# Optimization experiments

Hardware: AMD Instinct MI355X
Metric: run time of the kernel (lower is better)

## Reference

```python
import jax, jax.numpy as jnp
import numpy as np

N_NODES = 10000
N_EDGES = 160000
D = 128        # embedding_dim = in/out channels
E_DIM = 32     # edge feature dim
HEADS = 3
N_ETYPES = 64
ROUNDS = 2     # num_message_rounds
NEG_SLOPE = 0.2


def _lookup_maxnorm(table, idx):
    # torch Embedding(max_norm=1): rows with L2 norm > 1 are renormalized to norm 1
    v = table[idx]
    n = jnp.linalg.norm(v, axis=-1, keepdims=True)
    return v / jnp.maximum(n, 1.0)


def _edge_gat(x, src, dst, edge_attr, weight, att, euw, bias):
    # x: [N, D]; src/dst: [E] (self loops included); edge_attr: [E, E_DIM]
    N = x.shape[0]
    H = HEADS
    C = weight.shape[1] // H
    xh = (x @ weight).reshape(N, H, C)                 # [N, H, C]
    x_j = xh[src]                                      # gather source nodes  [E, H, C]
    x_i = xh[dst]                                      # gather target nodes  [E, H, C]
    ea = jnp.broadcast_to(edge_attr[:, None, :], (src.shape[0], H, edge_attr.shape[-1]))
    xj_cat = jnp.concatenate([x_j, ea], axis=-1)       # [E, H, C+E_DIM]
    # attention logits: (cat(x_i, x_j, e) * att).sum(-1)
    alpha = jnp.sum(jnp.concatenate([x_i, xj_cat], axis=-1) * att, axis=-1)  # [E, H]
    alpha = jax.nn.leaky_relu(alpha, NEG_SLOPE)
    # scatter-softmax over incoming edges of each dst node (stable)
    m = jax.ops.segment_max(alpha, dst, num_segments=N)        # [N, H]
    a = jnp.exp(alpha - m[dst])
    denom = jax.ops.segment_sum(a, dst, num_segments=N)        # [N, H]
    a = a / denom[dst]
    # weighted scatter-add aggregate
    aggr = jax.ops.segment_sum(xj_cat * a[..., None], dst, num_segments=N)  # [N, H, C+E_DIM]
    return aggr.mean(axis=1) @ euw + bias                       # [N, C]


def setup_inputs() -> dict:
    key = jax.random.key(0)
    ks = jax.random.split(key, 13)
    x_idx = jnp.arange(N_NODES, dtype=jnp.int32)
    src = jax.random.randint(ks[0], (N_EDGES,), 0, N_NODES, dtype=jnp.int32)
    off = jax.random.randint(ks[1], (N_EDGES,), 1, N_NODES, dtype=jnp.int32)
    dst = (src + off) % N_NODES    # guaranteed self-loop-free
    edge_index = jnp.stack([src, dst])
    edge_attr_idx = jax.random.randint(ks[2], (N_EDGES,), 0, N_ETYPES, dtype=jnp.int32)
    def g(k, shape):
        return jax.random.normal(k, shape, jnp.float32) * np.float32(np.sqrt(2.0 / sum(shape)))
    node_emb = g(ks[3], (N_NODES, D))
    edge_emb = g(ks[4], (N_ETYPES, E_DIM))
    w1 = g(ks[5], (D, HEADS * D))
    att1 = g(ks[6], (1, HEADS, 2 * D + E_DIM))
    euw1 = g(ks[7], (D + E_DIM, D))
    b1 = jnp.zeros((D,), jnp.float32)
    w2 = g(ks[8], (D, HEADS * D))
    att2 = g(ks[9], (1, HEADS, 2 * D + E_DIM))
    euw2 = g(ks[10], (D + E_DIM, D))
    b2 = jnp.zeros((D,), jnp.float32)
    return dict(x_idx=x_idx, edge_index=edge_index, edge_attr_idx=edge_attr_idx,
                node_emb=node_emb, edge_emb=edge_emb,
                w1=w1, att1=att1, euw1=euw1, b1=b1,
                w2=w2, att2=att2, euw2=euw2, b2=b2)


def reference(x_idx, edge_index, edge_attr_idx, node_emb, edge_emb,
              w1, att1, euw1, b1, w2, att2, euw2, b2):
    N = node_emb.shape[0]
    src0, dst0 = edge_index[0], edge_index[1]
    loop = jnp.arange(N, dtype=src0.dtype)
    src = jnp.concatenate([src0, loop])
    dst = jnp.concatenate([dst0, loop])
    x = _lookup_maxnorm(node_emb, x_idx)               # [N, D]
    ea = edge_emb[edge_attr_idx]                       # [E0, E_DIM]
    ea_full = jnp.concatenate([ea, jnp.zeros((N, ea.shape[-1]), ea.dtype)], axis=0)
    for _ in range(ROUNDS):
        # eval mode: dropout is identity
        x = jax.nn.elu(_edge_gat(x, src, dst, ea_full, w1, att1, euw1, b1))
        x = _edge_gat(x, src, dst, ea_full, w2, att2, euw2, b2)
    return x
```

## Files before the change

### kernel.cpp

```cpp
#include <hip/hip_runtime.h>
#include <hip/hip_bf16.h>

typedef __hip_bfloat16 bf16;
typedef __attribute__((ext_vector_type(8))) short short8;
typedef __attribute__((ext_vector_type(4))) float f32x4;
typedef __attribute__((ext_vector_type(4), aligned(4))) int i32x4u;
typedef __attribute__((ext_vector_type(4))) int i32x4;

__device__ __forceinline__ float b2f(bf16 v) { return __bfloat162float(v); }
__device__ __forceinline__ float2 i2f2(int w) {
  float lo = __uint_as_float(((unsigned)w) << 16);
  float hi = __uint_as_float(((unsigned)w) & 0xFFFF0000u);
  return make_float2(lo, hi);
}
__device__ __forceinline__ unsigned f2bfb(float f) {
  unsigned u = __float_as_uint(f);
  unsigned r = 0x7FFFu + ((u >> 16) & 1u);
  return (u + r) >> 16;
}
__device__ __forceinline__ unsigned pk2(float a, float b) {
  return f2bfb(a) | (f2bfb(b) << 16);
}
__device__ __forceinline__ float ldv(const void* p, int i, int f) {
  return f ? ((const float*)p)[i] : b2f(((const bf16*)p)[i]);
// ... 120 lines not shown
  if (hi > N) hi = N;
  int s = 0;
  for (int i = lo; i < hi; ++i) s += counts[i] + 1;
  int lane = t & 63, wv = t >> 6;
  int incl = s;
#pragma unroll
  for (int d = 1; d < 64; d <<= 1) {
    int u = __shfl_up(incl, d);
    if (lane >= d) incl += u;
  }
  if (lane == 63) wsum[wv] = incl;
  __syncthreads();
  if (t == 0) {
    int run = 0;
#pragma unroll
    for (int w = 0; w < 16; ++w) { int c = wsum[w]; wsum[w] = run; run += c; }
  }
  __syncthreads();
  int run = incl - s + wsum[wv];
  for (int i = lo; i < hi; ++i) {
    int c = counts[i] + 1;
    row_ptr[i] = run;
    counts[i] = run;
    run += c;
  }
  if (t == 1023) row_ptr[N] = run;
}

__global__ __launch_bounds__(256) void scatter_kernel(
    const int* __restrict__ src, const int* __restrict__ dst,
    const int* __restrict__ et, int* __restrict__ cursor,
    int* __restrict__ packed, int E0, int N) {
  int E = E0 + N;
  int i = blockIdx.x * blockDim.x + threadIdx.x;
  if (i < E0) {
    int d = dst[i];
    if ((unsigned)d >= (unsigned)N) d = 0;
    int p = atomicAdd(&cursor[d], 1);
    if ((unsigned)p >= (unsigned)E) p = 0;
    int t = et[i] & 63;
    packed[p] = (src[i] & 0xFFFF) | (t << 16);
  } else if (i < E) {
    int n = i - E0;
    int p = atomicAdd(&cursor[n], 1);
    if ((unsigned)p >= (unsigned)E) p = 0;
    packed[p] = (n & 0xFFFF) | (64 << 16);
  }
}

__global__ __launch_bounds__(384) void gemm_xh_s_mfma(
    const bf16* __restrict__ x, const bf16* __restrict__ WT,
    const float* __restrict__ attf, bf16* __restrict__ xh,
    float* __restrict__ s_i, float* __restrict__ s_j, int N) {
  __shared__ bf16 stage[32 * SH];
  __shared__ float lds_i[6][32];
  __shared__ float lds_j[6][32];
  int wave = threadIdx.x >> 6, lane = threadIdx.x & 63;
  int row_base = blockIdx.x * 32;
  int quad = lane >> 4, r16 = lane & 15;
  int rowA = row_base + r16;      if (rowA >= N) rowA = N - 1;
  int rowB = row_base + 16 + r16; if (rowB >= N) rowB = N - 1;
  const short8* apA = (const short8*)(x + (size_t)rowA * 128 + quad * 8);
  const short8* apB = (const short8*)(x + (size_t)rowB * 128 + quad * 8);
  short8 aA[4], aB[4];
#pragma unroll
  for (int kk = 0; kk < 4; ++kk) { aA[kk] = apA[kk * 4]; aB[kk] = apB[kk * 4]; }

  float piA[4] = {0.f, 0.f, 0.f, 0.f}, pjA[4] = {0.f, 0.f, 0.f, 0.f};
  float piB[4] = {0.f, 0.f, 0.f, 0.f}, pjB[4] = {0.f, 0.f, 0.f, 0.f};
#pragma unroll
  for (int j = 0; j < 4; ++j) {
    int col = wave * 64 + j * 16 + r16;
    const short8* bp = (const short8*)(WT + (size_t)col * 128 + quad * 8);
    short8 b[4];
#pragma unroll
    for (int kk = 0; kk < 4; ++kk) b[kk] = bp[kk * 4];
    f32x4 accA = {0.f, 0.f, 0.f, 0.f};
    f32x4 accB = {0.f, 0.f, 0.f, 0.f};
#pragma unroll
    for (int kk = 0; kk < 4; ++kk) {
      accA = __builtin_amdgcn_mfma_f32_16x16x32_bf16(aA[kk], b[kk], accA, 0, 0, 0);
      accB = __builtin_amdgcn_mfma_f32_16x16x32_bf16(aB[kk], b[kk], accB, 0, 0, 0);
    }
    int h = col >> 7, fi = col & 127, pair = fi >> 1, sub = fi & 1;
    int base = pair * 6 + h * 2 + sub;
#pragma unroll
    for (int r = 0; r < 4; ++r) {
      stage[(quad * 4 + r) * SH + base] = __float2bfloat16(accA[r]);
      stage[(16 + quad * 4 + r) * SH + base] = __float2bfloat16(accB[r]);
    }
    float ai = attf[h * 288 + fi];
    float aj = attf[h * 288 + 128 + fi];
#pragma unroll
    for (int r = 0; r < 4; ++r) {
      piA[r] = fmaf(accA[r], ai, piA[r]);
      pjA[r] = fmaf(accA[r], aj, pjA[r]);
      piB[r] = fmaf(accB[r], ai, piB[r]);
      pjB[r] = fmaf(accB[r], aj, pjB[r]);
    }
  }
#pragma unroll
  for (int d = 1; d < 16; d <<= 1) {
#pragma unroll
    for (int r = 0; r < 4; ++r) {
      piA[r] += __shfl_xor(piA[r], d);
      pjA[r] += __shfl_xor(pjA[r], d);
      piB[r] += __shfl_xor(piB[r], d);
      pjB[r] += __shfl_xor(pjB[r], d);
    }
  }
  if (r16 == 0) {
#pragma unroll
    for (int r = 0; r < 4; ++r) {
      lds_i[wave][quad * 4 + r] = piA[r];
      lds_j[wave][quad * 4 + r] = pjA[r];
      lds_i[wave][16 + quad * 4 + r] = piB[r];
      lds_j[wave][16 + quad * 4 + r] = pjB[r];
    }
  }
  __syncthreads();
  int m = threadIdx.x;
  if (m < 96) {
    int h = m / 32, r = m % 32;
    int node = row_base + r;
    if (node < N) s_i[node * 3 + h] = lds_i[2 * h][r] + lds_i[2 * h + 1][r];
  } else if (m < 192) {
    int tt = m - 96;
    int h = tt / 32, r = tt % 32;
    int node = row_base + r;
    if (node < N) s_j[node * 3 + h] = lds_j[2 * h][r] + lds_j[2 * h + 1][r];
  }
#pragma unroll
  for (int k = 0; k < 4; ++k) {
    int c = threadIdx.x + k * 384;
    int r = c / 48, o = c % 48;
    int node = row_base + r;
    if (node < N)
      *(i32x4*)(xh + (size_t)node * 384 + o * 8) =
          *(const i32x4*)(stage + r * SH + o * 8);
  }
}

__global__ __launch_bounds__(384) void fox_kernel(
    const bf16* __restrict__ aggr, const bf16* __restrict__ euwT,
    const float* __restrict__ biasf, int do_elu,
    const bf16* __restrict__ WT, const float* __restrict__ attf,
    bf16* __restrict__ xh, float* __restrict__ s_i, float* __restrict__ s_j,
    int N) {
  __shared__ bf16 xtile[16][136];
  __shared__ bf16 stage[16 * SH];
  __shared__ float lds_i[6][16];
  __shared__ float lds_j[6][16];
  int wave = threadIdx.x >> 6, lane = threadIdx.x & 63;
  int quad = lane >> 4, r16 = lane & 15;
  int row_base = blockIdx.x * 16;
  int row = row_base + r16; if (row >= N) row = N - 1;

  const short8* ap = (const short8*)(aggr + (size_t)row * 160 + quad * 8);
  short8 aa[5];
#pragma unroll
  for (int kk = 0; kk < 5; ++kk) aa[kk] = ap[kk * 4];
  for (int t = wave; t < 8; t += 6) {
    int col = t * 16 + r16;
    const short8* bp = (const short8*)(euwT + (size_t)col * 160 + quad * 8);
    f32x4 acc = {0.f, 0.f, 0.f, 0.f};
#pragma unroll
    for (int kk = 0; kk < 5; ++kk)
      acc = __builtin_amdgcn_mfma_f32_16x16x32_bf16(aa[kk], bp[kk * 4], acc, 0, 0, 0);
    float bv = biasf[col];
#pragma unroll
    for (int r = 0; r < 4; ++r) {
      float v = acc[r] + bv;
      if (do_elu) v = v > 0.0f ? v : expm1f(v);
      xtile[quad * 4 + r][col] = __float2bfloat16(v);
    }
  }
  __syncthreads();

  short8 a[4];
#pragma unroll
  for (int kk = 0; kk < 4; ++kk)
    a[kk] = *(const short8*)(&xtile[r16][quad * 8 + kk * 32]);

  float pi_r[4] = {0.f, 0.f, 0.f, 0.f};
  float pj_r[4] = {0.f, 0.f, 0.f, 0.f};
#pragma unroll
  for (int j = 0; j < 4; ++j) {
    int col = wave * 64 + j * 16 + r16;
    const short8* bp = (const short8*)(WT + (size_t)col * 128 + quad * 8);
    f32x4 acc = {0.f, 0.f, 0.f, 0.f};
#pragma unroll
    for (int kk = 0; kk < 4; ++kk)
      acc = __builtin_amdgcn_mfma_f32_16x16x32_bf16(a[kk], bp[kk * 4], acc, 0, 0, 0);
    int h = col >> 7, fi = col & 127, pair = fi >> 1, sub = fi & 1;
    int base = pair * 6 + h * 2 + sub;
#pragma unroll
    for (int r = 0; r < 4; ++r)
      stage[(quad * 4 + r) * SH + base] = __float2bfloat16(acc[r]);
    float ai = attf[h * 288 + fi];
    float aj = attf[h * 288 + 128 + fi];
#pragma unroll
    for (int r = 0; r < 4; ++r) {
      pi_r[r] = fmaf(acc[r], ai, pi_r[r]);
      pj_r[r] = fmaf(acc[r], aj, pj_r[r]);
    }
  }
#pragma unroll
  for (int d = 1; d < 16; d <<= 1) {
#pragma unroll
    for (int r = 0; r < 4; ++r) {
      pi_r[r] += __shfl_xor(pi_r[r], d);
      pj_r[r] += __shfl_xor(pj_r[r], d);
    }
  }
  if (r16 == 0) {
#pragma unroll
    for (int r = 0; r < 4; ++r) {
      lds_i[wave][quad * 4 + r] = pi_r[r];
      lds_j[wave][quad * 4 + r] = pj_r[r];
    }
  }
  __syncthreads();
  int m = threadIdx.x;
  if (m < 48) {
    int h = m / 16, r = m % 16;
    int node = row_base + r;
    if (node < N) s_i[node * 3 + h] = lds_i[2 * h][r] + lds_i[2 * h + 1][r];
  } else if (m < 96) {
    int tt = m - 48;
    int h = tt / 16, r = tt % 16;
    int node = row_base + r;
    if (node < N) s_j[node * 3 + h] = lds_j[2 * h][r] + lds_j[2 * h + 1][r];
  }
#pragma unroll
  for (int k = 0; k < 2; ++k) {
    int c = threadIdx.x + k * 384;
    int r = c / 48, o = c % 48;
    int node = row_base + r;
    if (node < N)
      *(i32x4*)(xh + (size_t)node * 384 + o * 8) =
          *(const i32x4*)(stage + r * SH + o * 8);
  }
}

__global__ __launch_bounds__(256) void edge_aggr_kernel(
    const int* __restrict__ xh_i, const float* __restrict__ s_i,
    const float* __restrict__ s_j, const float* __restrict__ s_et,
    const float2* __restrict__ eef2, const int* __restrict__ row_ptr,
    const int* __restrict__ packed, unsigned* __restrict__ aggr_u,
    int N, int E) {
  __shared__ float lds[2][512];
  int wid = threadIdx.x >> 6, lane = threadIdx.x & 63;
  int nodeLocal = wid >> 1, w = wid & 1;
  int n0 = blockIdx.x * 2 + nodeLocal;
  int n = n0 < N ? n0 : N - 1;
  int start = row_ptr[n], end = row_ptr[n + 1];
  if (start < 0) start = 0;
  if (start > E) start = E;
  if (end < start) end = start;
  if (end > E) end = E;
  int deg = end - start;
  float si0 = s_i[n * 3 + 0], si1 = s_i[n * 3 + 1], si2 = s_i[n * 3 + 2];

  float p0r = 0.f, p1r = 0.f, p2r = 0.f;
  int pkr = 0;
  float dp0 = 0.0f, dp1 = 0.0f, dp2 = 0.0f;
  int slot = 2 * lane + w;
  if (slot < deg) {
    int p = packed[start + slot];
    int s = p & 0xFFFF; if (s >= N) s = N - 1;
    int t = (p >> 16) & 127; if (t > 64) t = 64;
    float a0 = si0 + s_j[s * 3 + 0] + s_et[t * 3 + 0];
    float a1 = si1 + s_j[s * 3 + 1] + s_et[t * 3 + 1];
    float a2 = si2 + s_j[s * 3 + 2] + s_et[t * 3 + 2];
    a0 = a0 > 0.0f ? a0 : 0.2f * a0;
    a1 = a1 > 0.0f ? a1 : 0.2f * a1;
    a2 = a2 > 0.0f ? a2 : 0.2f * a2;
    a0 = fminf(fmaxf(a0, -60.0f), 60.0f);
    a1 = fminf(fmaxf(a1, -60.0f), 60.0f);
    a2 = fminf(fmaxf(a2, -60.0f), 60.0f);
    p0r = __expf(a0); p1r = __expf(a1); p2r = __expf(a2);
    dp0 = p0r; dp1 = p1r; dp2 = p2r;
    pkr = s | (t << 16);
  }
#pragma unroll
  for (int d = 32; d > 0; d >>= 1) {
    dp0 += __shfl_xor(dp0, d);
    dp1 += __shfl_xor(dp1, d);
    dp2 += __shfl_xor(dp2, d);
  }
  float d0 = dp0, d1 = dp1, d2 = dp2;

  float2 ax0 = make_float2(0.f, 0.f), ax1 = ax0, ax2 = ax0;
  float2 ae0 = ax0, ae1 = ax0, ae2 = ax0;
  int capped = deg < 128 ? deg : 128;
  int cnt = (capped > w) ? ((capped - w + 1) >> 1) : 0;

  {
    int j = 0;
    for (; j + 2 <= cnt; j += 2) {
      int pkA = __shfl(pkr, j), pkB = __shfl(pkr, j + 1);
      float qA0 = __shfl(p0r, j), qB0 = __shfl(p0r, j + 1);
      float qA1 = __shfl(p1r, j), qB1 = __shfl(p1r, j + 1);
      float qA2 = __shfl(p2r, j), qB2 = __shfl(p2r, j + 1);
      int sA = pkA & 0xFFFF, tA = pkA >> 16;
      int sB = pkB & 0xFFFF, tB = pkB >> 16;
      i32x4u qA = *(const i32x4u*)(xh_i + (size_t)sA * 192 + lane * 3);
      i32x4u qB = *(const i32x4u*)(xh_i + (size_t)sB * 192 + lane * 3);
      float2 vA0 = i2f2(qA.x), vA1 = i2f2(qA.y), vA2 = i2f2(qA.z);
      float2 vB0 = i2f2(qB.x), vB1 = i2f2(qB.y), vB2 = i2f2(qB.z);
      ax0.x = fmaf(qA0, vA0.x, ax0.x); ax0.y = fmaf(qA0, vA0.y, ax0.y);
      ax1.x = fmaf(qA1, vA1.x, ax1.x); ax1.y = fmaf(qA1, vA1.y, ax1.y);
      ax2.x = fmaf(qA2, vA2.x, ax2.x); ax2.y = fmaf(qA2, vA2.y, ax2.y);
      ax0.x = fmaf(qB0, vB0.x, ax0.x); ax0.y = fmaf(qB0, vB0.y, ax0.y);
      ax1.x = fmaf(qB1, vB1.x, ax1.x); ax1.y = fmaf(qB1, vB1.y, ax1.y);
      ax2.x = fmaf(qB2, vB2.x, ax2.x); ax2.y = fmaf(qB2, vB2.y, ax2.y);
      if (lane < 16) {
        if (tA != 64) {
          float2 ev = eef2[tA * 16 + lane];
          ae0.x = fmaf(qA0, ev.x, ae0.x); ae0.y = fmaf(qA0, ev.y, ae0.y);
          ae1.x = fmaf(qA1, ev.x, ae1.x); ae1.y = fmaf(qA1, ev.y, ae1.y);
          ae2.x = fmaf(qA2, ev.x, ae2.x); ae2.y = fmaf(qA2, ev.y, ae2.y);
        }
        if (tB != 64) {
          float2 ev = eef2[tB * 16 + lane];
          ae0.x = fmaf(qB0, ev.x, ae0.x); ae0.y = fmaf(qB0, ev.y, ae0.y);
          ae1.x = fmaf(qB1, ev.x, ae1.x); ae1.y = fmaf(qB1, ev.y, ae1.y);
          ae2.x = fmaf(qB2, ev.x, ae2.x); ae2.y = fmaf(qB2, ev.y, ae2.y);
        }
      }
    }
    if (j < cnt) {
      int pkA = __shfl(pkr, j);
      float qA0 = __shfl(p0r, j), qA1 = __shfl(p1r, j), qA2 = __shfl(p2r, j);
      int sA = pkA & 0xFFFF, tA = pkA >> 16;
      i32x4u qA = *(const i32x4u*)(xh_i + (size_t)sA * 192 + lane * 3);
      float2 vA0 = i2f2(qA.x), vA1 = i2f2(qA.y), vA2 = i2f2(qA.z);
      ax0.x = fmaf(qA0, vA0.x, ax0.x); ax0.y = fmaf(qA0, vA0.y, ax0.y);
      ax1.x = fmaf(qA1, vA1.x, ax1.x); ax1.y = fmaf(qA1, vA1.y, ax1.y);
      ax2.x = fmaf(qA2, vA2.x, ax2.x); ax2.y = fmaf(qA2, vA2.y, ax2.y);
      if (lane < 16 && tA != 64) {
        float2 ev = eef2[tA * 16 + lane];
        ae0.x = fmaf(qA0, ev.x, ae0.x); ae0.y = fmaf(qA0, ev.y, ae0.y);
        ae1.x = fmaf(qA1, ev.x, ae1.x); ae1.y = fmaf(qA1, ev.y, ae1.y);
        ae2.x = fmaf(qA2, ev.x, ae2.x); ae2.y = fmaf(qA2, ev.y, ae2.y);
      }
    }
  }

  if (w == 0) {
    for (int e = start + 128; e < end; ++e) {
      int p = packed[e];
      int s = p & 0xFFFF; if (s >= N) s = N - 1;
      int t = (p >> 16) & 127; if (t > 64) t = 64;
      float a0 = si0 + s_j[s * 3 + 0] + s_et[t * 3 + 0];
      float a1 = si1 + s_j[s * 3 + 1] + s_et[t * 3 + 1];
      float a2 = si2 + s_j[s * 3 + 2] + s_et[t * 3 + 2];
      a0 = a0 > 0.0f ? a0 : 0.2f * a0;
      a1 = a1 > 0.0f ? a1 : 0.2f * a1;
      a2 = a2 > 0.0f ? a2 : 0.2f * a2;
      a0 = fminf(fmaxf(a0, -60.0f), 60.0f);
      a1 = fminf(fmaxf(a1, -60.0f), 60.0f);
      a2 = fminf(fmaxf(a2, -60.0f), 60.0f);
      float p0 = __expf(a0), p1 = __expf(a1), p2 = __expf(a2);
      d0 += p0; d1 += p1; d2 += p2;
      i32x4u q = *(const i32x4u*)(xh_i + (size_t)s * 192 + lane * 3);
      float2 v0 = i2f2(q.x), v1 = i2f2(q.y), v2 = i2f2(q.z);
      ax0.x = fmaf(p0, v0.x, ax0.x); ax0.y = fmaf(p0, v0.y, ax0.y);
      ax1.x = fmaf(p1, v1.x, ax1.x); ax1.y = fmaf(p1, v1.y, ax1.y);
      ax2.x = fmaf(p2, v2.x, ax2.x); ax2.y = fmaf(p2, v2.y, ax2.y);
      if (t != 64 && lane < 16) {
        float2 ev = eef2[t * 16 + lane];
        ae0.x = fmaf(p0, ev.x, ae0.x); ae0.y = fmaf(p0, ev.y, ae0.y);
        ae1.x = fmaf(p1, ev.x, ae1.x); ae1.y = fmaf(p1, ev.y, ae1.y);
        ae2.x = fmaf(p2, ev.x, ae2.x); ae2.y = fmaf(p2, ev.y, ae2.y);
      }
    }
  }

  float* L = lds[nodeLocal];
  if (w == 1) {
    L[lane * 2 + 0] = ax0.x;       L[lane * 2 + 1] = ax0.y;
    L[128 + lane * 2 + 0] = ax1.x; L[128 + lane * 2 + 1] = ax1.y;
    L[256 + lane * 2 + 0] = ax2.x; L[256 + lane * 2 + 1] = ax2.y;
    if (lane < 16) {
      L[384 + lane * 2 + 0] = ae0.x; L[384 + lane * 2 + 1] = ae0.y;
      L[416 + lane * 2 + 0] = ae1.x; L[416 + lane * 2 + 1] = ae1.y;
      L[448 + lane * 2 + 0] = ae2.x; L[448 + lane * 2 + 1] = ae2.y;
    }
    if (lane == 0) { L[480] = d0; L[481] = d1; L[482] = d2; }
  }
  __syncthreads();
  if (w == 0 && n0 < N) {
    ax0.x += L[lane * 2 + 0];       ax0.y += L[lane * 2 + 1];
    ax1.x += L[128 + lane * 2 + 0]; ax1.y += L[128 + lane * 2 + 1];
    ax2.x += L[256 + lane * 2 + 0]; ax2.y += L[256 + lane * 2 + 1];
    if (lane < 16) {
      ae0.x += L[384 + lane * 2 + 0]; ae0.y += L[384 + lane * 2 + 1];
      ae1.x += L[416 + lane * 2 + 0]; ae1.y += L[416 + lane * 2 + 1];
      ae2.x += L[448 + lane * 2 + 0]; ae2.y += L[448 + lane * 2 + 1];
    }
    d0 += L[480]; d1 += L[481]; d2 += L[482];
    const float third = 1.0f / 3.0f;
    float i0 = third / fmaxf(d0, 1e-30f);
    float i1 = third / fmaxf(d1, 1e-30f);
    float i2 = third / fmaxf(d2, 1e-30f);
    aggr_u[(size_t)n0 * 80 + lane] =
        pk2(ax0.x * i0 + ax1.x * i1 + ax2.x * i2,
            ax0.y * i0 + ax1.y * i1 + ax2.y * i2);
    if (lane < 16)
      aggr_u[(size_t)n0 * 80 + 64 + lane] =
          pk2(ae0.x * i0 + ae1.x * i1 + ae2.x * i2,
              ae0.y * i0 + ae1.y * i1 + ae2.y * i2);
  }
}

__global__ __launch_bounds__(256) void gemm_out_mfma(
    const bf16* __restrict__ aggr, const bf16* __restrict__ euwT,
    const float* __restrict__ biasf, void* __restrict__ dout,
    const int* __restrict__ flag, int N) {
  int wave = threadIdx.x >> 6, lane = threadIdx.x & 63;
  int row_base = blockIdx.x * 16;
  int col_base = blockIdx.y * 64 + wave * 16;
  int quad = lane >> 4, r16 = lane & 15;
  int row = row_base + r16; if (row >= N) row = N - 1;
  int col = col_base + r16;
  f32x4 acc = {0.f, 0.f, 0.f, 0.f};
  const short8* ap = (const short8*)(aggr + (size_t)row * 160 + quad * 8);
  const short8* bp = (const short8*)(euwT + (size_t)col * 160 + quad * 8);
#pragma unroll
  for (int kk = 0; kk < 5; ++kk) {
    short8 a = ap[kk * 4];
    short8 b = bp[kk * 4];
    acc = __builtin_amdgcn_mfma_f32_16x16x32_bf16(a, b, acc, 0, 0, 0);
  }
  float bv = biasf[col];
  int f = *flag;
#pragma unroll
  for (int r = 0; r < 4; ++r) {
    int node = row_base + quad * 4 + r;
    if (node < N) {
      float v = acc[r] + bv;
      if (f) ((float*)dout)[(size_t)node * 128 + col] = v;
      else   ((bf16*)dout)[(size_t)node * 128 + col] = __float2bfloat16(v);
    }
  }
}

extern "C" void kernel_launch(void* const* d_in, const int* in_sizes, int n_in,
                              void* d_out, int out_size, void* d_ws, size_t ws_size,
                              hipStream_t stream) {
  const int* x_idx = (const int*)d_in[0];
  const int* edge_index = (const int*)d_in[1];
  const int* edge_attr_idx = (const int*)d_in[2];

  int N = in_sizes[0];
  int E0 = in_sizes[1] / 2;
  int E = E0 + N;
  const int* src = edge_index;
  const int* dst = edge_index + E0;

  size_t off = 0;
  char* base = (char*)d_ws;
  auto carve = [&](size_t bytes) -> void* {
    void* p = base + off;
    off += (bytes + 255) & ~(size_t)255;
    return p;
  };
  int* flag     = (int*)carve(256);
  int* counts   = (int*)carve((size_t)N * 4);
  int* row_ptr  = (int*)carve((size_t)(N + 1) * 4);
  int* packed   = (int*)carve((size_t)E * 4);
  float* s_i    = (float*)carve((size_t)N * 3 * 4);
  float* s_j    = (float*)carve((size_t)N * 3 * 4);
  float* s_et   = (float*)carve(2 * 65 * 3 * 4);
  float* eef    = (float*)carve(2048 * 4);
  float* att1f  = (float*)carve(864 * 4);
  float* att2f  = (float*)carve(864 * 4);
  float* b1f    = (float*)carve(128 * 4);
  float* b2f_   = (float*)carve(128 * 4);
  bf16* WT1     = (bf16*)carve(49152 * 2);
  bf16* WT2     = (bf16*)carve(49152 * 2);
  bf16* euT1    = (bf16*)carve(20480 * 2);
  bf16* euT2    = (bf16*)carve(20480 * 2);
  bf16* xh      = (bf16*)carve((size_t)N * 384 * 2 + 64);
  bf16* aggr    = (bf16*)carve((size_t)N * 160 * 2);
  bf16* xb      = (bf16*)d_out;
  (void)n_in; (void)out_size; (void)ws_size;

  wconv_kernel<<<(143296 + N + 255) / 256, 256, 0, stream>>>(
      d_in[4], d_in[5], d_in[6], d_in[7], d_in[8], d_in[9], d_in[10], d_in[11],
      d_in[12], flag, eef, att1f, att2f, b1f, b2f_, WT1, WT2, euT1, euT2,
      s_et, counts, N);
  int nb4 = (N + 3) / 4;
  prep_kernel<<<nb4, 256, 0, stream>>>(x_idx, d_in[3], flag, xb, counts, dst,
                                       E0, N);
  scan_kernel<<<1, 1024, 0, stream>>>(counts, row_ptr, N);
  scatter_kernel<<<(E + 255) / 256, 256, 0, stream>>>(src, dst, edge_attr_idx,
                                                      counts, packed, E0, N);

  int nrb16 = (N + 15) / 16;
  int nrb32 = (N + 31) / 32;
  int nb2 = (N + 1) / 2;

  gemm_xh_s_mfma<<<nrb32, 384, 0, stream>>>(xb, WT1, att1f, xh, s_i, s_j, N);
  edge_aggr_kernel<<<nb2, 256, 0, stream>>>(
      (const int*)xh, s_i, s_j, s_et, (const float2*)eef,
      row_ptr, packed, (unsigned*)aggr, N, E);
  fox_kernel<<<nrb16, 384, 0, stream>>>(aggr, euT1, b1f, 1, WT2, att2f,
                                        xh, s_i, s_j, N);
  edge_aggr_kernel<<<nb2, 256, 0, stream>>>(
      (const int*)xh, s_i, s_j, s_et + 195, (const float2*)eef,
      row_ptr, packed, (unsigned*)aggr, N, E);
  fox_kernel<<<nrb16, 384, 0, stream>>>(aggr, euT2, b2f_, 0, WT1, att1f,
                                        xh, s_i, s_j, N);
  edge_aggr_kernel<<<nb2, 256, 0, stream>>>(
      (const int*)xh, s_i, s_j, s_et, (const float2*)eef,
      row_ptr, packed, (unsigned*)aggr, N, E);
  fox_kernel<<<nrb16, 384, 0, stream>>>(aggr, euT1, b1f, 1, WT2, att2f,
                                        xh, s_i, s_j, N);
  edge_aggr_kernel<<<nb2, 256, 0, stream>>>(
      (const int*)xh, s_i, s_j, s_et + 195, (const float2*)eef,
      row_ptr, packed, (unsigned*)aggr, N, E);
  gemm_out_mfma<<<dim3(nrb16, 2), 256, 0, stream>>>(aggr, euT2, b2f_,
                                                    d_out, flag, N);
}
```

Baseline: 315.3 us.

## Fuse edge aggregation with following node GEMMs into one kernel per layer

Merges the per-node edge softmax aggregation with the subsequent euw projection, ELU and next-layer W GEMM (or the final output GEMM) into a single kernel. The aggregated features stay in shared memory instead of round-tripping through a global aggr buffer. To make this safe, xh and the s_i/s_j buffers are double-buffered across layers. Each wave now handles two nodes sequentially with one wave per node instead of two waves per node, which may reduce latency hiding on high-degree nodes and lowers grid parallelism.

```diff
diff --git a/kernel.cpp b/kernel.cpp
--- a/kernel.cpp
+++ b/kernel.cpp
@@ -196,7 +196,7 @@
     const bf16* __restrict__ x, const bf16* __restrict__ WT,
     const float* __restrict__ attf, bf16* __restrict__ xh,
     float* __restrict__ s_i, float* __restrict__ s_j, int N) {
-  __shared__ bf16 stage[32 * SH];
+  __shared__ __align__(16) bf16 stage[32 * SH];
   __shared__ float lds_i[6][32];
   __shared__ float lds_j[6][32];
   int wave = threadIdx.x >> 6, lane = threadIdx.x & 63;
@@ -285,27 +285,169 @@
   }
 }
 
-__global__ __launch_bounds__(384) void fox_kernel(
-    const bf16* __restrict__ aggr, const bf16* __restrict__ euwT,
-    const float* __restrict__ biasf, int do_elu,
-    const bf16* __restrict__ WT, const float* __restrict__ attf,
-    bf16* __restrict__ xh, float* __restrict__ s_i, float* __restrict__ s_j,
-    int N) {
+#define AGGR_NODE_BODY(n_, start_, deg_)                                      \
+  float2 ax0 = make_float2(0.f, 0.f), ax1 = ax0, ax2 = ax0;                   \
+  float2 ae0 = ax0, ae1 = ax0, ae2 = ax0;                                     \
+  float d0 = 0.f, d1 = 0.f, d2 = 0.f;                                         \
+  {                                                                           \
+    float si0 = s_i[(n_) * 3 + 0], si1 = s_i[(n_) * 3 + 1],                   \
+          si2 = s_i[(n_) * 3 + 2];                                            \
+    for (int c0 = 0; c0 < (deg_); c0 += 64) {                                 \
+      int mm = (deg_) - c0; if (mm > 64) mm = 64;                             \
+      float p0r = 0.f, p1r = 0.f, p2r = 0.f; int pkr = 0;                     \
+      if (lane < mm) {                                                        \
+        int p = packed[(start_) + c0 + lane];                                 \
+        int s = p & 0xFFFF; if (s >= N) s = N - 1;                            \
+        int t = (p >> 16) & 127; if (t > 64) t = 64;                          \
+        float a0 = si0 + s_j[s * 3 + 0] + s_et[t * 3 + 0];                    \
+        float a1 = si1 + s_j[s * 3 + 1] + s_et[t * 3 + 1];                    \
+        float a2 = si2 + s_j[s * 3 + 2] + s_et[t * 3 + 2];                    \
+        a0 = a0 > 0.0f ? a0 : 0.2f * a0;                                      \
+        a1 = a1 > 0.0f ? a1 : 0.2f * a1;                                      \
+        a2 = a2 > 0.0f ? a2 : 0.2f * a2;                                      \
+        a0 = fminf(fmaxf(a0, -60.0f), 60.0f);                                 \
+        a1 = fminf(fmaxf(a1, -60.0f), 60.0f);                                 \
+        a2 = fminf(fmaxf(a2, -60.0f), 60.0f);                                 \
+        p0r = __expf(a0); p1r = __expf(a1); p2r = __expf(a2);                 \
+        pkr = s | (t << 16);                                                  \
+      }                                                                       \
+      float dp0 = p0r, dp1 = p1r, dp2 = p2r;                                  \
+      _Pragma("unroll")                                                       \
+      for (int d = 32; d > 0; d >>= 1) {                                      \
+        dp0 += __shfl_xor(dp0, d);                                            \
+        dp1 += __shfl_xor(dp1, d);                                            \
+        dp2 += __shfl_xor(dp2, d);                                            \
+      }                                                                       \
+      d0 += dp0; d1 += dp1; d2 += dp2;                                        \
+      int j = 0;                                                              \
+      for (; j + 4 <= mm; j += 4) {                                           \
+        int pkA = __shfl(pkr, j), pkB = __shfl(pkr, j + 1);                   \
+        int pkC = __shfl(pkr, j + 2), pkD = __shfl(pkr, j + 3);               \
+        float qA0 = __shfl(p0r, j), qB0 = __shfl(p0r, j + 1);                 \
+        float qC0 = __shfl(p0r, j + 2), qD0 = __shfl(p0r, j + 3);             \
+        float qA1 = __shfl(p1r, j), qB1 = __shfl(p1r, j + 1);                 \
+        float qC1 = __shfl(p1r, j + 2), qD1 = __shfl(p1r, j + 3);             \
+        float qA2 = __shfl(p2r, j), qB2 = __shfl(p2r, j + 1);                 \
+        float qC2 = __shfl(p2r, j + 2), qD2 = __shfl(p2r, j + 3);             \
+        int sA = pkA & 0xFFFF, tA = pkA >> 16;                                \
+        int sB = pkB & 0xFFFF, tB = pkB >> 16;                                \
+        int sC = pkC & 0xFFFF, tC = pkC >> 16;                                \
+        int sD = pkD & 0xFFFF, tD = pkD >> 16;                                \
+        i32x4u qA = *(const i32x4u*)(xh_i + (size_t)sA * 192 + lane * 3);     \
+        i32x4u qB = *(const i32x4u*)(xh_i + (size_t)sB * 192 + lane * 3);     \
+        i32x4u qC = *(const i32x4u*)(xh_i + (size_t)sC * 192 + lane * 3);     \
+        i32x4u qD = *(const i32x4u*)(xh_i + (size_t)sD * 192 + lane * 3);     \
+        float2 vA0 = i2f2(qA.x), vA1 = i2f2(qA.y), vA2 = i2f2(qA.z);          \
+        float2 vB0 = i2f2(qB.x), vB1 = i2f2(qB.y), vB2 = i2f2(qB.z);          \
+        float2 vC0 = i2f2(qC.x), vC1 = i2f2(qC.y), vC2 = i2f2(qC.z);          \
+        float2 vD0 = i2f2(qD.x), vD1 = i2f2(qD.y), vD2 = i2f2(qD.z);          \
+        ax0.x = fmaf(qA0, vA0.x, ax0.x); ax0.y = fmaf(qA0, vA0.y, ax0.y);     \
+        ax1.x = fmaf(qA1, vA1.x, ax1.x); ax1.y = fmaf(qA1, vA1.y, ax1.y);     \
+        ax2.x = fmaf(qA2, vA2.x, ax2.x); ax2.y = fmaf(qA2, vA2.y, ax2.y);     \
+        ax0.x = fmaf(qB0, vB0.x, ax0.x); ax0.y = fmaf(qB0, vB0.y, ax0.y);     \
+        ax1.x = fmaf(qB1, vB1.x, ax1.x); ax1.y = fmaf(qB1, vB1.y, ax1.y);     \
+        ax2.x = fmaf(qB2, vB2.x, ax2.x); ax2.y = fmaf(qB2, vB2.y, ax2.y);     \
+        ax0.x = fmaf(qC0, vC0.x, ax0.x); ax0.y = fmaf(qC0, vC0.y, ax0.y);     \
+        ax1.x = fmaf(qC1, vC1.x, ax1.x); ax1.y = fmaf(qC1, vC1.y, ax1.y);     \
+        ax2.x = fmaf(qC2, vC2.x, ax2.x); ax2.y = fmaf(qC2, vC2.y, ax2.y);     \
+        ax0.x = fmaf(qD0, vD0.x, ax0.x); ax0.y = fmaf(qD0, vD0.y, ax0.y);     \
+        ax1.x = fmaf(qD1, vD1.x, ax1.x); ax1.y = fmaf(qD1, vD1.y, ax1.y);     \
+        ax2.x = fmaf(qD2, vD2.x, ax2.x); ax2.y = fmaf(qD2, vD2.y, ax2.y);     \
+        if (lane < 16) {                                                      \
+          if (tA != 64) {                                                     \
+            float2 ev = eef2[tA * 16 + lane];                                 \
+            ae0.x = fmaf(qA0, ev.x, ae0.x); ae0.y = fmaf(qA0, ev.y, ae0.y);   \
+            ae1.x = fmaf(qA1, ev.x, ae1.x); ae1.y = fmaf(qA1, ev.y, ae1.y);   \
+            ae2.x = fmaf(qA2, ev.x, ae2.x); ae2.y = fmaf(qA2, ev.y, ae2.y);   \
+          }                                                                   \
+          if (tB != 64) {                                                     \
+            float2 ev = eef2[tB * 16 + lane];                                 \
+            ae0.x = fmaf(qB0, ev.x, ae0.x); ae0.y = fmaf(qB0, ev.y, ae0.y);   \
+            ae1.x = fmaf(qB1, ev.x, ae1.x); ae1.y = fmaf(qB1, ev.y, ae1.y);   \
+            ae2.x = fmaf(qB2, ev.x, ae2.x); ae2.y = fmaf(qB2, ev.y, ae2.y);   \
+          }                                                                   \
+          if (tC != 64) {                                                     \
+            float2 ev = eef2[tC * 16 + lane];                                 \
+            ae0.x = fmaf(qC0, ev.x, ae0.x); ae0.y = fmaf(qC0, ev.y, ae0.y);   \
+            ae1.x = fmaf(qC1, ev.x, ae1.x); ae1.y = fmaf(qC1, ev.y, ae1.y);   \
+            ae2.x = fmaf(qC2, ev.x, ae2.x); ae2.y = fmaf(qC2, ev.y, ae2.y);   \
+          }                                                                   \
+          if (tD != 64) {                                                     \
+            float2 ev = eef2[tD * 16 + lane];                                 \
+            ae0.x = fmaf(qD0, ev.x, ae0.x); ae0.y = fmaf(qD0, ev.y, ae0.y);   \
+            ae1.x = fmaf(qD1, ev.x, ae1.x); ae1.y = fmaf(qD1, ev.y, ae1.y);   \
+            ae2.x = fmaf(qD2, ev.x, ae2.x); ae2.y = fmaf(qD2, ev.y, ae2.y);   \
+          }                                                                   \
+        }                                                                     \
+      }                                                                       \
+      for (; j < mm; ++j) {                                                   \
+        int pkA = __shfl(pkr, j);                                             \
+        float qA0 = __shfl(p0r, j), qA1 = __shfl(p1r, j), qA2 = __shfl(p2r, j);\
+        int sA = pkA & 0xFFFF, tA = pkA >> 16;                                \
+        i32x4u qA = *(const i32x4u*)(xh_i + (size_t)sA * 192 + lane * 3);     \
+        float2 vA0 = i2f2(qA.x), vA1 = i2f2(qA.y), vA2 = i2f2(qA.z);          \
+        ax0.x = fmaf(qA0, vA0.x, ax0.x); ax0.y = fmaf(qA0, vA0.y, ax0.y);     \
+        ax1.x = fmaf(qA1, vA1.x, ax1.x); ax1.y = fmaf(qA1, vA1.y, ax1.y);     \
+        ax2.x = fmaf(qA2, vA2.x, ax2.x); ax2.y = fmaf(qA2, vA2.y, ax2.y);     \
+        if (lane < 16 && tA != 64) {                                          \
+          float2 ev = eef2[tA * 16 + lane];                                   \
+          ae0.x = fmaf(qA0, ev.x, ae0.x); ae0.y = fmaf(qA0, ev.y, ae0.y);     \
+          ae1.x = fmaf(qA1, ev.x, ae1.x); ae1.y = fmaf(qA1, ev.y, ae1.y);     \
+          ae2.x = fmaf(qA2, ev.x, ae2.x); ae2.y = fmaf(qA2, ev.y, ae2.y);     \
+        }                                                                     \
+      }                                                                       \
+    }                                                                         \
+  }
+
+__global__ __launch_bounds__(512) void edge_fox_kernel(
+    const int* __restrict__ xh_i, const float* __restrict__ s_i,
+    const float* __restrict__ s_j, const float* __restrict__ s_et,
+    const float2* __restrict__ eef2, const int* __restrict__ row_ptr,
+    const int* __restrict__ packed,
+    const bf16* __restrict__ euwT, const float* __restrict__ biasf,
+    int do_elu, const bf16* __restrict__ WT, const float* __restrict__ attf,
+    bf16* __restrict__ xh_o, float* __restrict__ s_io,
+    float* __restrict__ s_jo, int N, int E) {
+  __shared__ __align__(16) bf16 atile[16][168];
   __shared__ bf16 xtile[16][136];
-  __shared__ bf16 stage[16 * SH];
+  __shared__ __align__(16) bf16 stage[16 * SH];
   __shared__ float lds_i[6][16];
   __shared__ float lds_j[6][16];
   int wave = threadIdx.x >> 6, lane = threadIdx.x & 63;
   int quad = lane >> 4, r16 = lane & 15;
   int row_base = blockIdx.x * 16;
-  int row = row_base + r16; if (row >= N) row = N - 1;
-
-  const short8* ap = (const short8*)(aggr + (size_t)row * 160 + quad * 8);
+
+  const float third = 1.0f / 3.0f;
+#pragma unroll 1
+  for (int u = 0; u < 2; ++u) {
+    int r = wave * 2 + u;
+    int n0 = row_base + r;
+    int n = n0 < N ? n0 : N - 1;
+    int start = row_ptr[n], end = row_ptr[n + 1];
+    if (start < 0) start = 0;
+    if (start > E) start = E;
+    if (end < start) end = start;
+    if (end > E) end = E;
+    int deg = end - start;
+    AGGR_NODE_BODY(n, start, deg)
+    float i0 = third / fmaxf(d0, 1e-30f);
+    float i1 = third / fmaxf(d1, 1e-30f);
+    float i2 = third / fmaxf(d2, 1e-30f);
+    unsigned* arow = (unsigned*)(&atile[r][0]);
+    arow[lane] = pk2(ax0.x * i0 + ax1.x * i1 + ax2.x * i2,
+                     ax0.y * i0 + ax1.y * i1 + ax2.y * i2);
+    if (lane < 16)
+      arow[64 + lane] = pk2(ae0.x * i0 + ae1.x * i1 + ae2.x * i2,
+                            ae0.y * i0 + ae1.y * i1 + ae2.y * i2);
+  }
+  __syncthreads();
+
   short8 aa[5];
 #pragma unroll
-  for (int kk = 0; kk < 5; ++kk) aa[kk] = ap[kk * 4];
-  for (int t = wave; t < 8; t += 6) {
-    int col = t * 16 + r16;
+  for (int kk = 0; kk < 5; ++kk)
+    aa[kk] = *(const short8*)(&atile[r16][quad * 8 + kk * 32]);
+  {
+    int col = wave * 16 + r16;
     const short8* bp = (const short8*)(euwT + (size_t)col * 160 + quad * 8);
     f32x4 acc = {0.f, 0.f, 0.f, 0.f};
 #pragma unroll
@@ -321,47 +463,49 @@
   }
   __syncthreads();
 
-  short8 a[4];
-#pragma unroll
-  for (int kk = 0; kk < 4; ++kk)
-    a[kk] = *(const short8*)(&xtile[r16][quad * 8 + kk * 32]);
-
-  float pi_r[4] = {0.f, 0.f, 0.f, 0.f};
-  float pj_r[4] = {0.f, 0.f, 0.f, 0.f};
-#pragma unroll
-  for (int j = 0; j < 4; ++j) {
-    int col = wave * 64 + j * 16 + r16;
-    const short8* bp = (const short8*)(WT + (size_t)col * 128 + quad * 8);
-    f32x4 acc = {0.f, 0.f, 0.f, 0.f};
+  if (wave < 6) {
+    short8 a[4];
 #pragma unroll
     for (int kk = 0; kk < 4; ++kk)
-      acc = __builtin_amdgcn_mfma_f32_16x16x32_bf16(a[kk], bp[kk * 4], acc, 0, 0, 0);
-    int h = col >> 7, fi = col & 127, pair = fi >> 1, sub = fi & 1;
-    int base = pair * 6 + h * 2 + sub;
-#pragma unroll
-    for (int r = 0; r < 4; ++r)
-      stage[(quad * 4 + r) * SH + base] = __float2bfloat16(acc[r]);
-    float ai = attf[h * 288 + fi];
-    float aj = attf[h * 288 + 128 + fi];
-#pragma unroll
-    for (int r = 0; r < 4; ++r) {
-      pi_r[r] = fmaf(acc[r], ai, pi_r[r]);
-      pj_r[r] = fmaf(acc[r], aj, pj_r[r]);
-    }
-  }
-#pragma unroll
-  for (int d = 1; d < 16; d <<= 1) {
-#pragma unroll
-    for (int r = 0; r < 4; ++r) {
-      pi_r[r] += __shfl_xor(pi_r[r], d);
-      pj_r[r] += __shfl_xor(pj_r[r], d);
-    }
-  }
-  if (r16 == 0) {
-#pragma unroll
-    for (int r = 0; r < 4; ++r) {
-      lds_i[wave][quad * 4 + r] = pi_r[r];
-      lds_j[wave][quad * 4 + r] = pj_r[r];
+      a[kk] = *(const short8*)(&xtile[r16][quad * 8 + kk * 32]);
+
+    float pi_r[4] = {0.f, 0.f, 0.f, 0.f};
+    float pj_r[4] = {0.f, 0.f, 0.f, 0.f};
+#pragma unroll
+    for (int j = 0; j < 4; ++j) {
+      int col = wave * 64 + j * 16 + r16;
+      const short8* bp = (const short8*)(WT + (size_t)col * 128 + quad * 8);
+      f32x4 acc = {0.f, 0.f, 0.f, 0.f};
+#pragma unroll
+      for (int kk = 0; kk < 4; ++kk)
+        acc = __builtin_amdgcn_mfma_f32_16x16x32_bf16(a[kk], bp[kk * 4], acc, 0, 0, 0);
+      int h = col >> 7, fi = col & 127, pair = fi >> 1, sub = fi & 1;
+      int base = pair * 6 + h * 2 + sub;
+#pragma unroll
+      for (int r = 0; r < 4; ++r)
+        stage[(quad * 4 + r) * SH + base] = __float2bfloat16(acc[r]);
+      float ai = attf[h * 288 + fi];
+      float aj = attf[h * 288 + 128 + fi];
+#pragma unroll
+      for (int r = 0; r < 4; ++r) {
+        pi_r[r] = fmaf(acc[r], ai, pi_r[r]);
+        pj_r[r] = fmaf(acc[r], aj, pj_r[r]);
+      }
+    }
+#pragma unroll
+    for (int d = 1; d < 16; d <<= 1) {
+#pragma unroll
+      for (int r = 0; r < 4; ++r) {
+        pi_r[r] += __shfl_xor(pi_r[r], d);
+        pj_r[r] += __shfl_xor(pj_r[r], d);
+      }
+    }
+    if (r16 == 0) {
+#pragma unroll
+      for (int r = 0; r < 4; ++r) {
+        lds_i[wave][quad * 4 + r] = pi_r[r];
+        lds_j[wave][quad * 4 + r] = pj_r[r];
+      }
     }
   }
   __syncthreads();
@@ -369,215 +513,73 @@
   if (m < 48) {
     int h = m / 16, r = m % 16;
     int node = row_base + r;
-    if (node < N) s_i[node * 3 + h] = lds_i[2 * h][r] + lds_i[2 * h + 1][r];
+    if (node < N) s_io[node * 3 + h] = lds_i[2 * h][r] + lds_i[2 * h + 1][r];
   } else if (m < 96) {
     int tt = m - 48;
     int h = tt / 16, r = tt % 16;
     int node = row_base + r;
-    if (node < N) s_j[node * 3 + h] = lds_j[2 * h][r] + lds_j[2 * h + 1][r];
+    if (node < N) s_jo[node * 3 + h] = lds_j[2 * h][r] + lds_j[2 * h + 1][r];
   }
 #pragma unroll
   for (int k = 0; k < 2; ++k) {
-    int c = threadIdx.x + k * 384;
-    int r = c / 48, o = c % 48;
-    int node = row_base + r;
-    if (node < N)
-      *(i32x4*)(xh + (size_t)node * 384 + o * 8) =
-          *(const i32x4*)(stage + r * SH + o * 8);
-  }
-}
-
-__global__ __launch_bounds__(256) void edge_aggr_kernel(
+    int c = threadIdx.x + k * 512;
+    if (c < 768) {
+      int r = c / 48, o = c % 48;
+      int node = row_base + r;
+      if (node < N)
+        *(i32x4*)(xh_o + (size_t)node * 384 + o * 8) =
+            *(const i32x4*)(stage + r * SH + o * 8);
+    }
+  }
+}
+
+__global__ __launch_bounds__(512) void edge_out_kernel(
     const int* __restrict__ xh_i, const float* __restrict__ s_i,
     const float* __restrict__ s_j, const float* __restrict__ s_et,
     const float2* __restrict__ eef2, const int* __restrict__ row_ptr,
-    const int* __restrict__ packed, unsigned* __restrict__ aggr_u,
-    int N, int E) {
-  __shared__ float lds[2][512];
-  int wid = threadIdx.x >> 6, lane = threadIdx.x & 63;
-  int nodeLocal = wid >> 1, w = wid & 1;
-  int n0 = blockIdx.x * 2 + nodeLocal;
-  int n = n0 < N ? n0 : N - 1;
-  int start = row_ptr[n], end = row_ptr[n + 1];
-  if (start < 0) start = 0;
-  if (start > E) start = E;
-  if (end < start) end = start;
-  if (end > E) end = E;
-  int deg = end - start;
-  float si0 = s_i[n * 3 + 0], si1 = s_i[n * 3 + 1], si2 = s_i[n * 3 + 2];
-
-  float p0r = 0.f, p1r = 0.f, p2r = 0.f;
-  int pkr = 0;
-  float dp0 = 0.0f, dp1 = 0.0f, dp2 = 0.0f;
-  int slot = 2 * lane + w;
-  if (slot < deg) {
-    int p = packed[start + slot];
-    int s = p & 0xFFFF; if (s >= N) s = N - 1;
-    int t = (p >> 16) & 127; if (t > 64) t = 64;
-    float a0 = si0 + s_j[s * 3 + 0] + s_et[t * 3 + 0];
-    float a1 = si1 + s_j[s * 3 + 1] + s_et[t * 3 + 1];
-    float a2 = si2 + s_j[s * 3 + 2] + s_et[t * 3 + 2];
-    a0 = a0 > 0.0f ? a0 : 0.2f * a0;
-    a1 = a1 > 0.0f ? a1 : 0.2f * a1;
-    a2 = a2 > 0.0f ? a2 : 0.2f * a2;
-    a0 = fminf(fmaxf(a0, -60.0f), 60.0f);
-    a1 = fminf(fmaxf(a1, -60.0f), 60.0f);
-    a2 = fminf(fmaxf(a2, -60.0f), 60.0f);
-    p0r = __expf(a0); p1r = __expf(a1); p2r = __expf(a2);
-    dp0 = p0r; dp1 = p1r; dp2 = p2r;
-    pkr = s | (t << 16);
-  }
-#pragma unroll
-  for (int d = 32; d > 0; d >>= 1) {
-    dp0 += __shfl_xor(dp0, d);
-    dp1 += __shfl_xor(dp1, d);
-    dp2 += __shfl_xor(dp2, d);
-  }
-  float d0 = dp0, d1 = dp1, d2 = dp2;
-
-  float2 ax0 = make_float2(0.f, 0.f), ax1 = ax0, ax2 = ax0;
-  float2 ae0 = ax0, ae1 = ax0, ae2 = ax0;
-  int capped = deg < 128 ? deg : 128;
-  int cnt = (capped > w) ? ((capped - w + 1) >> 1) : 0;
-
-  {
-    int j = 0;
-    for (; j + 2 <= cnt; j += 2) {
-      int pkA = __shfl(pkr, j), pkB = __shfl(pkr, j + 1);
-      float qA0 = __shfl(p0r, j), qB0 = __shfl(p0r, j + 1);
-      float qA1 = __shfl(p1r, j), qB1 = __shfl(p1r, j + 1);
-      float qA2 = __shfl(p2r, j), qB2 = __shfl(p2r, j + 1);
-      int sA = pkA & 0xFFFF, tA = pkA >> 16;
-      int sB = pkB & 0xFFFF, tB = pkB >> 16;
-      i32x4u qA = *(const i32x4u*)(xh_i + (size_t)sA * 192 + lane * 3);
-      i32x4u qB = *(const i32x4u*)(xh_i + (size_t)sB * 192 + lane * 3);
-      float2 vA0 = i2f2(qA.x), vA1 = i2f2(qA.y), vA2 = i2f2(qA.z);
-      float2 vB0 = i2f2(qB.x), vB1 = i2f2(qB.y), vB2 = i2f2(qB.z);
-      ax0.x = fmaf(qA0, vA0.x, ax0.x); ax0.y = fmaf(qA0, vA0.y, ax0.y);
-      ax1.x = fmaf(qA1, vA1.x, ax1.x); ax1.y = fmaf(qA1, vA1.y, ax1.y);
-      ax2.x = fmaf(qA2, vA2.x, ax2.x); ax2.y = fmaf(qA2, vA2.y, ax2.y);
-      ax0.x = fmaf(qB0, vB0.x, ax0.x); ax0.y = fmaf(qB0, vB0.y, ax0.y);
-      ax1.x = fmaf(qB1, vB1.x, ax1.x); ax1.y = fmaf(qB1, vB1.y, ax1.y);
-      ax2.x = fmaf(qB2, vB2.x, ax2.x); ax2.y = fmaf(qB2, vB2.y, ax2.y);
-      if (lane < 16) {
-        if (tA != 64) {
-          float2 ev = eef2[tA * 16 + lane];
-          ae0.x = fmaf(qA0, ev.x, ae0.x); ae0.y = fmaf(qA0, ev.y, ae0.y);
-          ae1.x = fmaf(qA1, ev.x, ae1.x); ae1.y = fmaf(qA1, ev.y, ae1.y);
-          ae2.x = fmaf(qA2, ev.x, ae2.x); ae2.y = fmaf(qA2, ev.y, ae2.y);
-        }
-        if (tB != 64) {
-          float2 ev = eef2[tB * 16 + lane];
-          ae0.x = fmaf(qB0, ev.x, ae0.x); ae0.y = fmaf(qB0, ev.y, ae0.y);
-          ae1.x = fmaf(qB1, ev.x, ae1.x); ae1.y = fmaf(qB1, ev.y, ae1.y);
-          ae2.x = fmaf(qB2, ev.x, ae2.x); ae2.y = fmaf(qB2, ev.y, ae2.y);
-        }
-      }
-    }
-    if (j < cnt) {
-      int pkA = __shfl(pkr, j);
-      float qA0 = __shfl(p0r, j), qA1 = __shfl(p1r, j), qA2 = __shfl(p2r, j);
-      int sA = pkA & 0xFFFF, tA = pkA >> 16;
-      i32x4u qA = *(const i32x4u*)(xh_i + (size_t)sA * 192 + lane * 3);
-      float2 vA0 = i2f2(qA.x), vA1 = i2f2(qA.y), vA2 = i2f2(qA.z);
-      ax0.x = fmaf(qA0, vA0.x, ax0.x); ax0.y = fmaf(qA0, vA0.y, ax0.y);
-      ax1.x = fmaf(qA1, vA1.x, ax1.x); ax1.y = fmaf(qA1, vA1.y, ax1.y);
-      ax2.x = fmaf(qA2, vA2.x, ax2.x); ax2.y = fmaf(qA2, vA2.y, ax2.y);
-      if (lane < 16 && tA != 64) {
-        float2 ev = eef2[tA * 16 + lane];
-        ae0.x = fmaf(qA0, ev.x, ae0.x); ae0.y = fmaf(qA0, ev.y, ae0.y);
-        ae1.x = fmaf(qA1, ev.x, ae1.x); ae1.y = fmaf(qA1, ev.y, ae1.y);
-        ae2.x = fmaf(qA2, ev.x, ae2.x); ae2.y = fmaf(qA2, ev.y, ae2.y);
-      }
-    }
-  }
-
-  if (w == 0) {
-    for (int e = start + 128; e < end; ++e) {
-      int p = packed[e];
-      int s = p & 0xFFFF; if (s >= N) s = N - 1;
-      int t = (p >> 16) & 127; if (t > 64) t = 64;
-      float a0 = si0 + s_j[s * 3 + 0] + s_et[t * 3 + 0];
-      float a1 = si1 + s_j[s * 3 + 1] + s_et[t * 3 + 1];
-      float a2 = si2 + s_j[s * 3 + 2] + s_et[t * 3 + 2];
-      a0 = a0 > 0.0f ? a0 : 0.2f * a0;
-      a1 = a1 > 0.0f ? a1 : 0.2f * a1;
-      a2 = a2 > 0.0f ? a2 : 0.2f * a2;
-      a0 = fminf(fmaxf(a0, -60.0f), 60.0f);
-      a1 = fminf(fmaxf(a1, -60.0f), 60.0f);
-      a2 = fminf(fmaxf(a2, -60.0f), 60.0f);
-      float p0 = __expf(a0), p1 = __expf(a1), p2 = __expf(a2);
-      d0 += p0; d1 += p1; d2 += p2;
-      i32x4u q = *(const i32x4u*)(xh_i + (size_t)s * 192 + lane * 3);
-      float2 v0 = i2f2(q.x), v1 = i2f2(q.y), v2 = i2f2(q.z);
-      ax0.x = fmaf(p0, v0.x, ax0.x); ax0.y = fmaf(p0, v0.y, ax0.y);
-      ax1.x = fmaf(p1, v1.x, ax1.x); ax1.y = fmaf(p1, v1.y, ax1.y);
-      ax2.x = fmaf(p2, v2.x, ax2.x); ax2.y = fmaf(p2, v2.y, ax2.y);
-      if (t != 64 && lane < 16) {
-        float2 ev = eef2[t * 16 + lane];
-        ae0.x = fmaf(p0, ev.x, ae0.x); ae0.y = fmaf(p0, ev.y, ae0.y);
-        ae1.x = fmaf(p1, ev.x, ae1.x); ae1.y = fmaf(p1, ev.y, ae1.y);
-        ae2.x = fmaf(p2, ev.x, ae2.x); ae2.y = fmaf(p2, ev.y, ae2.y);
-      }
-    }
-  }
-
-  float* L = lds[nodeLocal];
-  if (w == 1) {
-    L[lane * 2 + 0] = ax0.x;       L[lane * 2 + 1] = ax0.y;
-    L[128 + lane * 2 + 0] = ax1.x; L[128 + lane * 2 + 1] = ax1.y;
-    L[256 + lane * 2 + 0] = ax2.x; L[256 + lane * 2 + 1] = ax2.y;
-    if (lane < 16) {
-      L[384 + lane * 2 + 0] = ae0.x; L[384 + lane * 2 + 1] = ae0.y;
-      L[416 + lane * 2 + 0] = ae1.x; L[416 + lane * 2 + 1] = ae1.y;
-      L[448 + lane * 2 + 0] = ae2.x; L[448 + lane * 2 + 1] = ae2.y;
-    }
-    if (lane == 0) { L[480] = d0; L[481] = d1; L[482] = d2; }
-  }
-  __syncthreads();
-  if (w == 0 && n0 < N) {
-    ax0.x += L[lane * 2 + 0];       ax0.y += L[lane * 2 + 1];
-    ax1.x += L[128 + lane * 2 + 0]; ax1.y += L[128 + lane * 2 + 1];
-    ax2.x += L[256 + lane * 2 + 0]; ax2.y += L[256 + lane * 2 + 1];
-    if (lane < 16) {
-      ae0.x += L[384 + lane * 2 + 0]; ae0.y += L[384 + lane * 2 + 1];
-      ae1.x += L[416 + lane * 2 + 0]; ae1.y += L[416 + lane * 2 + 1];
-      ae2.x += L[448 + lane * 2 + 0]; ae2.y += L[448 + lane * 2 + 1];
-    }
-    d0 += L[480]; d1 += L[481]; d2 += L[482];
-    const float third = 1.0f / 3.0f;
+    const int* __restrict__ packed,
+    const bf16* __restrict__ euwT, const float* __restrict__ biasf,
+    void* __restrict__ dout, const int* __restrict__ flag, int N, int E) {
+  __shared__ __align__(16) bf16 atile[16][168];
+  int wave = threadIdx.x >> 6, lane = threadIdx.x & 63;
+  int quad = lane >> 4, r16 = lane & 15;
+  int row_base = blockIdx.x * 16;
+
+  const float third = 1.0f / 3.0f;
+#pragma unroll 1
+  for (int u = 0; u < 2; ++u) {
+    int r = wave * 2 + u;
+    int n0 = row_base + r;
+    int n = n0 < N ? n0 : N - 1;
+    int start = row_ptr[n], end = row_ptr[n + 1];
+    if (start < 0) start = 0;
+    if (start > E) start = E;
+    if (end < start) end = start;
+    if (end > E) end = E;
+    int deg = end - start;
+    AGGR_NODE_BODY(n, start, deg)
     float i0 = third / fmaxf(d0, 1e-30f);
     float i1 = third / fmaxf(d1, 1e-30f);
     float i2 = third / fmaxf(d2, 1e-30f);
-    aggr_u[(size_t)n0 * 80 + lane] =
-        pk2(ax0.x * i0 + ax1.x * i1 + ax2.x * i2,
-            ax0.y * i0 + ax1.y * i1 + ax2.y * i2);
+    unsigned* arow = (unsigned*)(&atile[r][0]);
+    arow[lane] = pk2(ax0.x * i0 + ax1.x * i1 + ax2.x * i2,
+                     ax0.y * i0 + ax1.y * i1 + ax2.y * i2);
     if (lane < 16)
-      aggr_u[(size_t)n0 * 80 + 64 + lane] =
-          pk2(ae0.x * i0 + ae1.x * i1 + ae2.x * i2,
-              ae0.y * i0 + ae1.y * i1 + ae2.y * i2);
-  }
-}
-
-__global__ __launch_bounds__(256) void gemm_out_mfma(
-    const bf16* __restrict__ aggr, const bf16* __restrict__ euwT,
-    const float* __restrict__ biasf, void* __restrict__ dout,
-    const int* __restrict__ flag, int N) {
-  int wave = threadIdx.x >> 6, lane = threadIdx.x & 63;
-  int row_base = blockIdx.x * 16;
-  int col_base = blockIdx.y * 64 + wave * 16;
-  int quad = lane >> 4, r16 = lane & 15;
-  int row = row_base + r16; if (row >= N) row = N - 1;
-  int col = col_base + r16;
+      arow[64 + lane] = pk2(ae0.x * i0 + ae1.x * i1 + ae2.x * i2,
+                            ae0.y * i0 + ae1.y * i1 + ae2.y * i2);
+  }
+  __syncthreads();
+
+  short8 aa[5];
+#pragma unroll
+  for (int kk = 0; kk < 5; ++kk)
+    aa[kk] = *(const short8*)(&atile[r16][quad * 8 + kk * 32]);
+  int col = wave * 16 + r16;
+  const short8* bp = (const short8*)(euwT + (size_t)col * 160 + quad * 8);
   f32x4 acc = {0.f, 0.f, 0.f, 0.f};
-  const short8* ap = (const short8*)(aggr + (size_t)row * 160 + quad * 8);
-  const short8* bp = (const short8*)(euwT + (size_t)col * 160 + quad * 8);
-#pragma unroll
-  for (int kk = 0; kk < 5; ++kk) {
-    short8 a = ap[kk * 4];
-    short8 b = bp[kk * 4];
-    acc = __builtin_amdgcn_mfma_f32_16x16x32_bf16(a, b, acc, 0, 0, 0);
-  }
+#pragma unroll
+  for (int kk = 0; kk < 5; ++kk)
+    acc = __builtin_amdgcn_mfma_f32_16x16x32_bf16(aa[kk], bp[kk * 4], acc, 0, 0, 0);
   float bv = biasf[col];
   int f = *flag;
 #pragma unroll
@@ -615,8 +617,10 @@
   int* counts   = (int*)carve((size_t)N * 4);
   int* row_ptr  = (int*)carve((size_t)(N + 1) * 4);
   int* packed   = (int*)carve((size_t)E * 4);
-  float* s_i    = (float*)carve((size_t)N * 3 * 4);
-  float* s_j    = (float*)carve((size_t)N * 3 * 4);
+  float* s_iA   = (float*)carve((size_t)N * 3 * 4);
+  float* s_jA   = (float*)carve((size_t)N * 3 * 4);
+  float* s_iB   = (float*)carve((size_t)N * 3 * 4);
+  float* s_jB   = (float*)carve((size_t)N * 3 * 4);
   float* s_et   = (float*)carve(2 * 65 * 3 * 4);
   float* eef    = (float*)carve(2048 * 4);
   float* att1f  = (float*)carve(864 * 4);
@@ -627,8 +631,8 @@
   bf16* WT2     = (bf16*)carve(49152 * 2);
   bf16* euT1    = (bf16*)carve(20480 * 2);
   bf16* euT2    = (bf16*)carve(20480 * 2);
-  bf16* xh      = (bf16*)carve((size_t)N * 384 * 2 + 64);
-  bf16* aggr    = (bf16*)carve((size_t)N * 160 * 2);
+  bf16* xhA     = (bf16*)carve((size_t)N * 384 * 2 + 64);
+  bf16* xhB     = (bf16*)carve((size_t)N * 384 * 2 + 64);
   bf16* xb      = (bf16*)d_out;
   (void)n_in; (void)out_size; (void)ws_size;
 
@@ -645,27 +649,18 @@
 
   int nrb16 = (N + 15) / 16;
   int nrb32 = (N + 31) / 32;
-  int nb2 = (N + 1) / 2;
-
-  gemm_xh_s_mfma<<<nrb32, 384, 0, stream>>>(xb, WT1, att1f, xh, s_i, s_j, N);
-  edge_aggr_kernel<<<nb2, 256, 0, stream>>>(
-      (const int*)xh, s_i, s_j, s_et, (const float2*)eef,
-      row_ptr, packed, (unsigned*)aggr, N, E);
-  fox_kernel<<<nrb16, 384, 0, stream>>>(aggr, euT1, b1f, 1, WT2, att2f,
-                                        xh, s_i, s_j, N);
-  edge_aggr_kernel<<<nb2, 256, 0, stream>>>(
-      (const int*)xh, s_i, s_j, s_et + 195, (const float2*)eef,
-      row_ptr, packed, (unsigned*)aggr, N, E);
-  fox_kernel<<<nrb16, 384, 0, stream>>>(aggr, euT2, b2f_, 0, WT1, att1f,
-                                        xh, s_i, s_j, N);
-  edge_aggr_kernel<<<nb2, 256, 0, stream>>>(
-      (const int*)xh, s_i, s_j, s_et, (const float2*)eef,
-      row_ptr, packed, (unsigned*)aggr, N, E);
-  fox_kernel<<<nrb16, 384, 0, stream>>>(aggr, euT1, b1f, 1, WT2, att2f,
-                                        xh, s_i, s_j, N);
-  edge_aggr_kernel<<<nb2, 256, 0, stream>>>(
-      (const int*)xh, s_i, s_j, s_et + 195, (const float2*)eef,
-      row_ptr, packed, (unsigned*)aggr, N, E);
-  gemm_out_mfma<<<dim3(nrb16, 2), 256, 0, stream>>>(aggr, euT2, b2f_,
-                                                    d_out, flag, N);
-}
+
+  gemm_xh_s_mfma<<<nrb32, 384, 0, stream>>>(xb, WT1, att1f, xhA, s_iA, s_jA, N);
+  edge_fox_kernel<<<nrb16, 512, 0, stream>>>(
+      (const int*)xhA, s_iA, s_jA, s_et, (const float2*)eef, row_ptr, packed,
+      euT1, b1f, 1, WT2, att2f, xhB, s_iB, s_jB, N, E);
+  edge_fox_kernel<<<nrb16, 512, 0, stream>>>(
+      (const int*)xhB, s_iB, s_jB, s_et + 195, (const float2*)eef, row_ptr,
+      packed, euT2, b2f_, 0, WT1, att1f, xhA, s_iA, s_jA, N, E);
+  edge_fox_kernel<<<nrb16, 512, 0, stream>>>(
+      (const int*)xhA, s_iA, s_jA, s_et, (const float2*)eef, row_ptr, packed,
+      euT1, b1f, 1, WT2, att2f, xhB, s_iB, s_jB, N, E);
+  edge_out_kernel<<<nrb16, 512, 0, stream>>>(
+      (const int*)xhB, s_iB, s_jB, s_et + 195, (const float2*)eef, row_ptr,
+      packed, euT2, b2f_, d_out, flag, N, E);
+}
```

New measurement: 330.1 us. +4.7%, slower.
